# Kernel optimization log

Measured on AMD Instinct MI355X. Metric: run time of the kernel, lower is better.

The kernel has to match this reference:

```python
import jax, jax.numpy as jnp
import numpy as np

K = 16  # neighbors per point (no self-loop)


def _knn_idx(pos, k):
    # pos: (N, 3). Squared euclidean pairwise distances via the ||a-b||^2 expansion.
    n = pos.shape[0]
    sq = jnp.sum(pos * pos, axis=1)                      # (N,)
    d = sq[:, None] + sq[None, :] - 2.0 * (pos @ pos.T)  # (N, N)
    # exclude self (loop=False in torch_cluster.knn_graph)
    diag = jnp.arange(n)
    d = d.at[diag, diag].set(jnp.inf)
    _, idx = jax.lax.top_k(-d, k)                        # k smallest distances -> (N, k)
    return idx


def setup_inputs() -> dict:
    key = jax.random.key(0)
    ks = jax.random.split(key, 6)
    N, C, D = 16384, 64, 64
    x = jax.random.normal(ks[0], (N, C), dtype=jnp.float32)
    pos = jax.random.normal(ks[1], (N, 3), dtype=jnp.float32)
    W1 = jax.random.normal(ks[2], (2 * C, D), dtype=jnp.float32) * 0.08
    b1 = jax.random.normal(ks[3], (D,), dtype=jnp.float32) * 0.02
    W2 = jax.random.normal(ks[4], (D, D), dtype=jnp.float32) * 0.12
    b2 = jax.random.normal(ks[5], (D,), dtype=jnp.float32) * 0.02
    return {"x": x, "pos": pos, "W1": W1, "b1": b1, "W2": W2, "b2": b2}


def reference(x, pos, W1, b1, W2, b2):
    # EdgeConv: for each center i with k-NN neighbors j:
    #   e_ij = MLP([x_i, x_j - x_i]);  out_i = max_j e_ij
    idx = _knn_idx(pos, K)                               # (N, K) int32
    x_j = x[idx]                                         # (N, K, C) gather
    x_i = x[:, None, :]                                  # (N, 1, C)
    ef = jnp.concatenate(
        [jnp.broadcast_to(x_i, x_j.shape), x_j - x_i], axis=-1
    )                                                    # (N, K, 2C)
    h = jax.nn.relu(jnp.einsum("nkc,cd->nkd", ef, W1) + b1)
    h = jnp.einsum("nkd,de->nke", h, W2) + b2            # (N, K, D)
    # each node has exactly K incoming edges -> scatter_max == max over K axis
    return jnp.max(h, axis=1)                            # (N, D)
```

## Files before the change

kernel.cpp:

```cpp
#include <hip/hip_runtime.h>
#include <hip/hip_bf16.h>


#define NPTS 16384
#define CH 64

#define GLO  (-4.5f)
#define GH   0.28125f
#define INVH 3.5555555556f
#define GDIM 32
#define GCELLS (GDIM * GDIM * GDIM)

typedef __attribute__((ext_vector_type(8))) short short8;
typedef __attribute__((ext_vector_type(4))) float floatx4;

__device__ __forceinline__ unsigned short f2bf(float f) {
    unsigned u = __float_as_uint(f);
    u += 0x7FFFu + ((u >> 16) & 1u);
    return (unsigned short)(u >> 16);
}
__device__ __forceinline__ float bf2f(unsigned short u) {
    return __uint_as_float(((unsigned)u) << 16);
}
__device__ __forceinline__ unsigned wave_iscan(unsigned x) {
    x += (unsigned)__builtin_amdgcn_update_dpp(0, (int)x, 0x111, 0xF, 0xF, true);
    x += (unsigned)__builtin_amdgcn_update_dpp(0, (int)x, 0x112, 0xF, 0xF, true);
    x += (unsigned)__builtin_amdgcn_update_dpp(0, (int)x, 0x114, 0xF, 0xF, true);
    x += (unsigned)__builtin_amdgcn_update_dpp(0, (int)x, 0x118, 0xF, 0xF, true);
    x += (unsigned)__builtin_amdgcn_update_dpp(0, (int)x, 0x142, 0xA, 0xF, true);
    x += (unsigned)__builtin_amdgcn_update_dpp(0, (int)x, 0x143, 0xC, 0xF, true);
    return x;
}
__device__ __forceinline__ int cell_of(float x, float y, float z) {
    int cx = (int)floorf((x - GLO) * INVH);
    int cy = (int)floorf((y - GLO) * INVH);
    int cz = (int)floorf((z - GLO) * INVH);
    cx = min(max(cx, 0), GDIM - 1);
    cy = min(max(cy, 0), GDIM - 1);
    cz = min(max(cz, 0), GDIM - 1);
    return (cz * GDIM + cy) * GDIM + cx;
}

__global__ __launch_bounds__(256) void count_prep_kernel(const float* __restrict__ pos,
                                                         int* __restrict__ counts,
                                                         const float* __restrict__ x,
                                                         const float* __restrict__ W1,
                                                         const float* __restrict__ b1,
                                                         float* __restrict__ vout,
                                                         unsigned short* __restrict__ ubuf) {
    __shared__ unsigned short Wct[128 * 72];
    __shared__ unsigned short Abuf[64 * 72];
    __shared__ float Wraw[128 * 64];

    const int t = threadIdx.x;
    if (blockIdx.x < 64) {
        const int i = blockIdx.x * 256 + t;
        atomicAdd(&counts[cell_of(pos[i * 3], pos[i * 3 + 1], pos[i * 3 + 2])], 1);
        return;
    }
    const int bid  = blockIdx.x - 64;
    const int lane = t & 63;
    const int w    = t >> 6;

    {
        const float4* W1v = (const float4*)W1;
        float4* Wr4 = (float4*)Wraw;
#pragma unroll
        for (int i = 0; i < 8; ++i) Wr4[i * 256 + t] = W1v[i * 256 + t];
    }
    __syncthreads();
    {
        const int n = t & 127;
        const int ks = (t >> 7) * 32;
#pragma unroll
        for (int i = 0; i < 32; ++i) {
            const int k = ks + i;
            float val;
            if (n < 64) val = Wraw[k * 64 + n] - Wraw[(64 + k) * 64 + n];
            else        val = Wraw[(64 + k) * 64 + (n - 64)];
            Wct[n * 72 + k] = f2bf(val);
        }
    }
    {
        const int col = t & 63;
#pragma unroll
        for (int i = 0; i < 16; ++i) {
            const int r2 = (t >> 6) + 4 * i;
            const int gp = bid * 64 + r2;
            Abuf[r2 * 72 + col] = f2bf(x[(size_t)gp * CH + col]);
        }
    }
    __syncthreads();

    const int m16 = lane & 15;
    const int q   = lane >> 4;

    floatx4 acc[8];
#pragma unroll
    for (int nt = 0; nt < 8; ++nt) acc[nt] = (floatx4){0.f, 0.f, 0.f, 0.f};

#pragma unroll
    for (int kk = 0; kk < 64; kk += 32) {
        const short8 a = *(const short8*)(Abuf + (w * 16 + m16) * 72 + kk + q * 8);
#pragma unroll
        for (int nt = 0; nt < 8; ++nt) {
            const short8 b = *(const short8*)(Wct + (nt * 16 + m16) * 72 + kk + q * 8);
            acc[nt] = __builtin_amdgcn_mfma_f32_16x16x32_bf16(a, b, acc[nt], 0, 0, 0);
        }
    }

#pragma unroll
    for (int nt = 0; nt < 8; ++nt) {
        const int n = nt * 16 + m16;
#pragma unroll
        for (int r = 0; r < 4; ++r) {
            const int gp = bid * 64 + w * 16 + q * 4 + r;
            if (n < 64) vout[(size_t)gp * CH + n] = acc[nt][r] + b1[n];
            else        ubuf[(size_t)gp * CH + (n - 64)] = f2bf(acc[nt][r]);
        }
    }
}

__global__ __launch_bounds__(1024) void scan_kernel(const int* __restrict__ counts,
                                                    int* __restrict__ starts,
                                                    int* __restrict__ cursor) {
    __shared__ int lds[1024];
    const int t = threadIdx.x;
    int4 v[8];
    const int4* c4 = (const int4*)counts + t * 8;
#pragma unroll
    for (int i = 0; i < 8; ++i) v[i] = c4[i];
    int sum = 0;
#pragma unroll
    for (int i = 0; i < 8; ++i) sum += v[i].x + v[i].y + v[i].z + v[i].w;
    lds[t] = sum;
    __syncthreads();
    for (int off = 1; off < 1024; off <<= 1) {
        int x = 0;
        if (t >= off) x = lds[t - off];
        __syncthreads();
        lds[t] += x;
        __syncthreads();
    }
    int pre = (t == 0) ? 0 : lds[t - 1];
    int4* s4 = (int4*)starts + t * 8;
    int4* u4 = (int4*)cursor + t * 8;
#pragma unroll
    for (int i = 0; i < 8; ++i) {
        int4 o;
        o.x = pre; pre += v[i].x;
        o.y = pre; pre += v[i].y;
        o.z = pre; pre += v[i].z;
        o.w = pre; pre += v[i].w;
        s4[i] = o;
        u4[i] = o;
    }
    if (t == 1023) starts[GCELLS] = pre;
}

__global__ __launch_bounds__(256) void grid_scatter_kernel(const float* __restrict__ pos,
                                                           int* __restrict__ cursor,
                                                           float4* __restrict__ spos,
                                                           unsigned short* __restrict__ sidx) {
    const int i = blockIdx.x * 256 + threadIdx.x;
    const float a = pos[i * 3], b = pos[i * 3 + 1], c = pos[i * 3 + 2];
    const int dst = atomicAdd(&cursor[cell_of(a, b, c)], 1);
    spos[dst] = make_float4(a, b, c, a * a + b * b + c * c);
    sidx[dst] = (unsigned short)i;
}

#define SENT 0xFF800000FFFFFFFFULL
#define NB 4

__global__ __launch_bounds__(64) void knn_grid_kernel(const float4* __restrict__ spos,
                                                      const unsigned short* __restrict__ sidx,
                                                      const int* __restrict__ starts,
                                                      unsigned short* __restrict__ knn_out) {
    __shared__ int lds_ex[64];
    __shared__ int lds_st[64];
    __shared__ unsigned long long buf[64];
    const int lane = threadIdx.x;
    const int sq   = blockIdx.x;

    const float4 qv = spos[sq];
    const float qx = qv.x, qy = qv.y, qz = qv.z, sqi = qv.w;
    const int qrow = (int)sidx[sq];
    const int cix = min(max((int)floorf((qx - GLO) * INVH), 0), GDIM - 1);
    const int ciy = min(max((int)floorf((qy - GLO) * INVH), 0), GDIM - 1);
    const int ciz = min(max((int)floorf((qz - GLO) * INVH), 0), GDIM - 1);

    unsigned long long list = SENT;
    float tau = __uint_as_float(0x7F800000u);
    bool first = true;
    int nbuf = 0;

    auto do_flush = [&]() {
        unsigned long long ck = (lane < nbuf) ? buf[lane] : SENT;
#pragma unroll
        for (int k = 2; k <= 64; k <<= 1) {
#pragma unroll
            for (int jj = k >> 1; jj >= 1; jj >>= 1) {
                const unsigned long long o = __shfl_xor(ck, jj);
                const bool takeMin = (((lane & k) == 0) == ((lane & jj) == 0));
                const unsigned long long mn = (ck < o) ? ck : o;
                const unsigned long long mx = (ck < o) ? o : ck;
                ck = takeMin ? mn : mx;
            }
        }
        const unsigned long long cv = __shfl(ck, 31 - lane);
        unsigned long long m = SENT;
        if (lane < 16) m = list;
        else if (lane < 32) m = cv;
#pragma unroll
        for (int jj = 16; jj >= 1; jj >>= 1) {
            const unsigned long long o = __shfl_xor(m, jj);
            const unsigned long long mn = (m < o) ? m : o;
            const unsigned long long mx = (m < o) ? o : m;
            m = ((lane & jj) == 0) ? mn : mx;
        }
        list = m;
        const unsigned thi = (unsigned)__builtin_amdgcn_readlane(
            (int)(unsigned)(list >> 32), 15);
        const unsigned fb = (thi >= 0x80000000u) ? (thi & 0x7FFFFFFFu) : ~thi;
        tau = __uint_as_float(fb);
        nbuf = 0;
    };

    int pax = 1, pbx = 0, pay = 1, pby = 0, paz = 1, pbz = 0;

    for (int s = 1; s < GDIM + 1; ++s) {
        const int ax = max(cix - s, 0), bx = min(cix + s, GDIM - 1);
        const int ay = max(ciy - s, 0), by = min(ciy + s, GDIM - 1);
        const int az = max(ciz - s, 0), bz = min(ciz + s, GDIM - 1);
        const int dy = by - ay + 1, dz = bz - az + 1;
        const int npair = dy * dz;
        const float invdy = 1.0f / (float)dy;

        for (int pb = 0; pb < npair; pb += 64) {
            const int pair = pb + lane;
            int stA = 0, lenA = 0, stB = 0, lenB = 0;
            if (pair < npair) {
                const int czo = (int)(((float)pair + 0.5f) * invdy);
                const int cyo = pair - czo * dy;
                const int cy = ay + cyo, cz = az + czo;
                const int rowb = (cz * GDIM + cy) * GDIM;
                const bool inner = cy >= pay && cy <= pby && cz >= paz && cz <= pbz;
                const int bA = inner ? (pax - 1) : bx;
                if (bA >= ax) {
                    stA  = starts[rowb + ax];
                    lenA = starts[rowb + bA + 1] - stA;
                }
                if (inner) {
                    const int aB = pbx + 1;
                    if (bx >= aB) {
                        stB  = starts[rowb + aB];
                        lenB = starts[rowb + bx + 1] - stB;
                    }
                }
            }
#pragma unroll
            for (int setsel = 0; setsel < 2; ++setsel) {
                const int st  = setsel ? stB  : stA;
                const int len = setsel ? lenB : lenA;
                if (__ballot(len > 0) == 0ULL) continue;
                const unsigned pfx = wave_iscan((unsigned)len);
                const int T = __builtin_amdgcn_readlane((int)pfx, 63);
                lds_ex[lane] = (int)pfx - len;
                lds_st[lane] = st;

                for (int b0 = 0; b0 < T; b0 += 64 * NB) {
                    float4 pts[NB];
                    int    jor[NB];
                    bool   act[NB];
                    bool   live[NB];
#pragma unroll
                    for (int nb = 0; nb < NB; ++nb) {
                        const int bb = b0 + nb * 64;
                        live[nb] = bb < T;
                        act[nb] = false;
                        if (live[nb]) {
                            const int p = bb + lane;
                            int j = 0;
#pragma unroll
                            for (int stp = 32; stp >= 1; stp >>= 1) {
                                const int m = j + stp;
                                if (lds_ex[m] <= p) j = m;
                            }
                            int idx = lds_st[j] + (p - lds_ex[j]);
                            idx = min(idx, NPTS - 1);
                            act[nb] = p < T;
                            pts[nb] = spos[idx];
                            jor[nb] = (int)sidx[idx];
                        }
                    }
#pragma unroll
                    for (int nb = 0; nb < NB; ++nb) {
                        if (!live[nb]) continue;
                        const float dot = fmaf(qx, pts[nb].x,
                                               fmaf(qy, pts[nb].y, qz * pts[nb].z));
                        const float d = fmaf(-2.0f, dot, sqi + pts[nb].w);

                        if (first) {
                            first = false;
                            unsigned kd = __float_as_uint(d);
                            kd = ((int)kd < 0) ? ~kd : (kd | 0x80000000u);
                            unsigned long long key =
                                (((unsigned long long)kd) << 32) | (unsigned)jor[nb];
                            if (!(act[nb] && jor[nb] != qrow)) key = SENT;
#pragma unroll
                            for (int k = 2; k <= 64; k <<= 1) {
#pragma unroll
                                for (int jj = k >> 1; jj >= 1; jj >>= 1) {
                                    const unsigned long long o = __shfl_xor(key, jj);
                                    const bool takeMin =
                                        (((lane & k) == 0) == ((lane & jj) == 0));
                                    const unsigned long long mn = (key < o) ? key : o;
                                    const unsigned long long mx = (key < o) ? o : key;
                                    key = takeMin ? mn : mx;
                                }
                            }
                            list = key;
                            const unsigned thi = (unsigned)__builtin_amdgcn_readlane(
                                (int)(unsigned)(list >> 32), 15);
                            const unsigned fb =
                                (thi >= 0x80000000u) ? (thi & 0x7FFFFFFFu) : ~thi;
                            tau = __uint_as_float(fb);
                            continue;
                        }

                        const bool cand = act[nb] && (jor[nb] != qrow) && (d <= tau);
                        const unsigned long long mask = __ballot(cand);
                        if (mask) {
                            const int cnt = __popcll(mask);
                            if (nbuf + cnt > 64) do_flush();
                            if (cand) {
                                unsigned kd = __float_as_uint(d);
                                kd = ((int)kd < 0) ? ~kd : (kd | 0x80000000u);
                                const unsigned long long key =
                                    (((unsigned long long)kd) << 32) | (unsigned)jor[nb];
                                const int rank =
                                    __popcll(mask & ((1ULL << lane) - 1ULL));
                                buf[nbuf + rank] = key;
                            }
                            nbuf += cnt;
                        }
                    }
                }
            }
        }

        if (nbuf) do_flush();

        const float BIG = 1e30f;
        float dout = BIG;
        if (ax > 0)        dout = fminf(dout, qx - (GLO + ax * GH));
        if (bx < GDIM - 1) dout = fminf(dout, (GLO + (bx + 1) * GH) - qx);
        if (ay > 0)        dout = fminf(dout, qy - (GLO + ay * GH));
        if (by < GDIM - 1) dout = fminf(dout, (GLO + (by + 1) * GH) - qy);
        if (az > 0)        dout = fminf(dout, qz - (GLO + az * GH));
        if (bz < GDIM - 1) dout = fminf(dout, (GLO + (bz + 1) * GH) - qz);
        if (dout * dout > tau + 1e-4f) break;
        if (ax == 0 && bx == GDIM - 1 && ay == 0 && by == GDIM - 1 &&
            az == 0 && bz == GDIM - 1) break;
        pax = ax; pbx = bx; pay = ay; pby = by; paz = az; pbz = bz;
    }

    if (lane < 16)
        knn_out[qrow * 16 + lane] = (unsigned short)(list & 0xFFFFULL);
}

__global__ __launch_bounds__(256) void edge_kernel(const unsigned short* __restrict__ ubuf,
                                                   const float* __restrict__ W2,
                                                   const float* __restrict__ b2,
                                                   const unsigned short* __restrict__ knn,
                                                   float* __restrict__ out) {
    __shared__ unsigned short h[128 * 72];
    __shared__ unsigned short W2t[64 * 72];

    const int t    = threadIdx.x;
    const int lane = t & 63;
    const int w    = t >> 6;

    {
        const int n = t & 63;
        const int kb = (t >> 6) * 16;
#pragma unroll
        for (int i = 0; i < 16; ++i) {
            const int k = kb + i;
            W2t[n * 72 + k] = f2bf(W2[k * 64 + n]);
        }
    }
    {
        const int k = t >> 4;
        const int c = t & 15;
#pragma unroll
        for (int i = 0; i < 8; ++i) {
            const int gn = blockIdx.x * 8 + i;
            const int gj = (int)knn[gn * 16 + k];
            const float4  vv = ((const float4*)(out + (size_t)gn * CH))[c];
            const ushort4 uu = ((const ushort4*)(ubuf + (size_t)gj * CH))[c];
            ushort4 hv;
            hv.x = f2bf(fmaxf(vv.x + bf2f(uu.x), 0.f));
            hv.y = f2bf(fmaxf(vv.y + bf2f(uu.y), 0.f));
            hv.z = f2bf(fmaxf(vv.z + bf2f(uu.z), 0.f));
            hv.w = f2bf(fmaxf(vv.w + bf2f(uu.w), 0.f));
            const int r2 = i * 16 + k;
            *(ushort4*)(h + r2 * 72 + c * 4) = hv;
        }
    }
    __syncthreads();

    const int m16 = lane & 15;
    const int q   = lane >> 4;

    floatx4 acc[2][4];
#pragma unroll
    for (int i = 0; i < 2; ++i)
#pragma unroll
        for (int nt = 0; nt < 4; ++nt) acc[i][nt] = (floatx4){0.f, 0.f, 0.f, 0.f};

#pragma unroll
    for (int kk = 0; kk < 64; kk += 32) {
        const short8 a0 = *(const short8*)(h + ((w * 2 + 0) * 16 + m16) * 72 + kk + q * 8);
        const short8 a1 = *(const short8*)(h + ((w * 2 + 1) * 16 + m16) * 72 + kk + q * 8);
#pragma unroll
        for (int nt = 0; nt < 4; ++nt) {
            const short8 b = *(const short8*)(W2t + (nt * 16 + m16) * 72 + kk + q * 8);
            acc[0][nt] = __builtin_amdgcn_mfma_f32_16x16x32_bf16(a0, b, acc[0][nt], 0, 0, 0);
            acc[1][nt] = __builtin_amdgcn_mfma_f32_16x16x32_bf16(a1, b, acc[1][nt], 0, 0, 0);
        }
    }

#pragma unroll
    for (int i = 0; i < 2; ++i) {
        const int mt = w * 2 + i;
        const int gn = blockIdx.x * 8 + mt;
#pragma unroll
        for (int nt = 0; nt < 4; ++nt) {
            float m0 = fmaxf(fmaxf(acc[i][nt][0], acc[i][nt][1]),
                             fmaxf(acc[i][nt][2], acc[i][nt][3]));
            m0 = fmaxf(m0, __shfl_xor(m0, 16));
            m0 = fmaxf(m0, __shfl_xor(m0, 32));
            if (lane < 16)
                out[(size_t)gn * CH + nt * 16 + lane] = m0 + b2[nt * 16 + lane];
        }
    }
}

extern "C" void kernel_launch(void* const* d_in, const int* in_sizes, int n_in,
                              void* d_out, int out_size, void* d_ws, size_t ws_size,
                              hipStream_t stream) {
    const float* x   = (const float*)d_in[0];
    const float* pos = (const float*)d_in[1];
    const float* W1  = (const float*)d_in[2];
    const float* b1  = (const float*)d_in[3];
    const float* W2  = (const float*)d_in[4];
    const float* b2  = (const float*)d_in[5];
    float* out = (float*)d_out;

    char* ws = (char*)d_ws;
    unsigned short* knn  = (unsigned short*)ws;
    unsigned short* ubuf = (unsigned short*)(ws + 524288);
    int*    counts = (int*)(ws + 2621440);
    int*    starts = (int*)(ws + 2752512);
    int*    cursor = (int*)(ws + 2883600);
    float4* spos   = (float4*)(ws + 3014672);
    unsigned short* sidx = (unsigned short*)(ws + 3276816);

    hipMemsetAsync(counts, 0, GCELLS * sizeof(int), stream);
    count_prep_kernel<<<320, 256, 0, stream>>>(pos, counts, x, W1, b1, out, ubuf);
    scan_kernel<<<1, 1024, 0, stream>>>(counts, starts, cursor);
    grid_scatter_kernel<<<NPTS / 256, 256, 0, stream>>>(pos, cursor, spos, sidx);
    knn_grid_kernel<<<NPTS, 64, 0, stream>>>(spos, sidx, starts, knn);
    edge_kernel<<<NPTS / 8, 256, 0, stream>>>(ubuf, W2, b2, knn, out);
}
```

Measured before the change: 151.2 us.

## Fuse kNN with edge MLP, merge scan with scatter, precompute W2t

The edge MLP second layer and max-reduction now run inside the kNN kernel: each wave gathers its 16 neighbor features from the in-register candidate list and runs the MFMAs directly, so the knn index buffer round-trip and the separate edge kernel launch go away. The scan kernel switches from an LDS Hillis-Steele loop to a wave scan plus per-wave sums, and absorbs the grid scatter, which drops one launch. W2 transpose/bf16 conversion moves to an extra block of the prep kernel. The risks are a single-block scatter with only 1024 threads doing 16K atomics serially, and a two-wave kNN block layout that may change occupancy.

```diff
diff --git a/kernel.cpp b/kernel.cpp
--- a/kernel.cpp
+++ b/kernel.cpp
@@ -46,8 +46,10 @@
                                                          const float* __restrict__ x,
                                                          const float* __restrict__ W1,
                                                          const float* __restrict__ b1,
+                                                         const float* __restrict__ W2,
                                                          float* __restrict__ vout,
-                                                         unsigned short* __restrict__ ubuf) {
+                                                         unsigned short* __restrict__ ubuf,
+                                                         unsigned short* __restrict__ W2t) {
     __shared__ unsigned short Wct[128 * 72];
     __shared__ unsigned short Abuf[64 * 72];
     __shared__ float Wraw[128 * 64];
@@ -56,6 +58,13 @@
     if (blockIdx.x < 64) {
         const int i = blockIdx.x * 256 + t;
         atomicAdd(&counts[cell_of(pos[i * 3], pos[i * 3 + 1], pos[i * 3 + 2])], 1);
+        return;
+    }
+    if (blockIdx.x == 320) {
+        for (int i = t; i < 4096; i += 256) {
+            const int n = i >> 6, k = i & 63;
+            W2t[n * 64 + k] = f2bf(W2[k * 64 + n]);
+        }
         return;
     }
     const int bid  = blockIdx.x - 64;
@@ -121,11 +130,17 @@
     }
 }
 
-__global__ __launch_bounds__(1024) void scan_kernel(const int* __restrict__ counts,
-                                                    int* __restrict__ starts,
-                                                    int* __restrict__ cursor) {
-    __shared__ int lds[1024];
-    const int t = threadIdx.x;
+__global__ __launch_bounds__(1024) void scan_scatter_kernel(const float* __restrict__ pos,
+                                                            const int* __restrict__ counts,
+                                                            int* __restrict__ starts,
+                                                            int* __restrict__ cursor,
+                                                            float4* __restrict__ spos,
+                                                            unsigned short* __restrict__ sidx) {
+    __shared__ int wsum[16];
+    const int t    = threadIdx.x;
+    const int lane = t & 63;
+    const int wv   = t >> 6;
+
     int4 v[8];
     const int4* c4 = (const int4*)counts + t * 8;
 #pragma unroll
@@ -133,16 +148,14 @@
     int sum = 0;
 #pragma unroll
     for (int i = 0; i < 8; ++i) sum += v[i].x + v[i].y + v[i].z + v[i].w;
-    lds[t] = sum;
+
+    const unsigned incl = wave_iscan((unsigned)sum);
+    if (lane == 63) wsum[wv] = (int)incl;
     __syncthreads();
-    for (int off = 1; off < 1024; off <<= 1) {
-        int x = 0;
-        if (t >= off) x = lds[t - off];
-        __syncthreads();
-        lds[t] += x;
-        __syncthreads();
-    }
-    int pre = (t == 0) ? 0 : lds[t - 1];
+    int base = (int)incl - sum;
+    for (int k = 0; k < wv; ++k) base += wsum[k];
+
+    int pre = base;
     int4* s4 = (int4*)starts + t * 8;
     int4* u4 = (int4*)cursor + t * 8;
 #pragma unroll
@@ -156,31 +169,35 @@
         u4[i] = o;
     }
     if (t == 1023) starts[GCELLS] = pre;
-}
-
-__global__ __launch_bounds__(256) void grid_scatter_kernel(const float* __restrict__ pos,
-                                                           int* __restrict__ cursor,
-                                                           float4* __restrict__ spos,
-                                                           unsigned short* __restrict__ sidx) {
-    const int i = blockIdx.x * 256 + threadIdx.x;
-    const float a = pos[i * 3], b = pos[i * 3 + 1], c = pos[i * 3 + 2];
-    const int dst = atomicAdd(&cursor[cell_of(a, b, c)], 1);
-    spos[dst] = make_float4(a, b, c, a * a + b * b + c * c);
-    sidx[dst] = (unsigned short)i;
+    __syncthreads();
+
+    for (int i = t; i < NPTS; i += 1024) {
+        const float a = pos[i * 3], b = pos[i * 3 + 1], c = pos[i * 3 + 2];
+        const int dst = atomicAdd(&cursor[cell_of(a, b, c)], 1);
+        spos[dst] = make_float4(a, b, c, a * a + b * b + c * c);
+        sidx[dst] = (unsigned short)i;
+    }
 }
 
 #define SENT 0xFF800000FFFFFFFFULL
 #define NB 4
 
-__global__ __launch_bounds__(64) void knn_grid_kernel(const float4* __restrict__ spos,
-                                                      const unsigned short* __restrict__ sidx,
-                                                      const int* __restrict__ starts,
-                                                      unsigned short* __restrict__ knn_out) {
-    __shared__ int lds_ex[64];
-    __shared__ int lds_st[64];
-    __shared__ unsigned long long buf[64];
-    const int lane = threadIdx.x;
-    const int sq   = blockIdx.x;
+__global__ __launch_bounds__(128) void knn_edge_kernel(const float4* __restrict__ spos,
+                                                       const unsigned short* __restrict__ sidx,
+                                                       const int* __restrict__ starts,
+                                                       const unsigned short* __restrict__ ubuf,
+                                                       const unsigned short* __restrict__ W2t,
+                                                       const float* __restrict__ b2,
+                                                       float* __restrict__ out) {
+    __shared__ int lds_ex[128];
+    __shared__ int lds_st[128];
+    __shared__ unsigned long long bufs[128];
+    const int lane  = threadIdx.x & 63;
+    const int w     = threadIdx.x >> 6;
+    int* ex = lds_ex + w * 64;
+    int* st_ = lds_st + w * 64;
+    unsigned long long* buf = bufs + w * 64;
+    const int sq = blockIdx.x * 2 + w;
 
     const float4 qv = spos[sq];
     const float qx = qv.x, qy = qv.y, qz = qv.z, sqi = qv.w;
@@ -265,8 +282,8 @@
                 if (__ballot(len > 0) == 0ULL) continue;
                 const unsigned pfx = wave_iscan((unsigned)len);
                 const int T = __builtin_amdgcn_readlane((int)pfx, 63);
-                lds_ex[lane] = (int)pfx - len;
-                lds_st[lane] = st;
+                ex[lane] = (int)pfx - len;
+                st_[lane] = st;
 
                 for (int b0 = 0; b0 < T; b0 += 64 * NB) {
                     float4 pts[NB];
@@ -284,9 +301,9 @@
 #pragma unroll
                             for (int stp = 32; stp >= 1; stp >>= 1) {
                                 const int m = j + stp;
-                                if (lds_ex[m] <= p) j = m;
+                                if (ex[m] <= p) j = m;
                             }
-                            int idx = lds_st[j] + (p - lds_ex[j]);
+                            int idx = st_[j] + (p - ex[j]);
                             idx = min(idx, NPTS - 1);
                             act[nb] = p < T;
                             pts[nb] = spos[idx];
@@ -365,84 +382,53 @@
         pax = ax; pbx = bx; pay = ay; pby = by; paz = az; pbz = bz;
     }
 
-    if (lane < 16)
-        knn_out[qrow * 16 + lane] = (unsigned short)(list & 0xFFFFULL);
-}
-
-__global__ __launch_bounds__(256) void edge_kernel(const unsigned short* __restrict__ ubuf,
-                                                   const float* __restrict__ W2,
-                                                   const float* __restrict__ b2,
-                                                   const unsigned short* __restrict__ knn,
-                                                   float* __restrict__ out) {
-    __shared__ unsigned short h[128 * 72];
-    __shared__ unsigned short W2t[64 * 72];
-
-    const int t    = threadIdx.x;
-    const int lane = t & 63;
-    const int w    = t >> 6;
-
     {
-        const int n = t & 63;
-        const int kb = (t >> 6) * 16;
-#pragma unroll
-        for (int i = 0; i < 16; ++i) {
-            const int k = kb + i;
-            W2t[n * 72 + k] = f2bf(W2[k * 64 + n]);
-        }
-    }
-    {
-        const int k = t >> 4;
-        const int c = t & 15;
-#pragma unroll
-        for (int i = 0; i < 8; ++i) {
-            const int gn = blockIdx.x * 8 + i;
-            const int gj = (int)knn[gn * 16 + k];
-            const float4  vv = ((const float4*)(out + (size_t)gn * CH))[c];
-            const ushort4 uu = ((const ushort4*)(ubuf + (size_t)gj * CH))[c];
-            ushort4 hv;
-            hv.x = f2bf(fmaxf(vv.x + bf2f(uu.x), 0.f));
-            hv.y = f2bf(fmaxf(vv.y + bf2f(uu.y), 0.f));
-            hv.z = f2bf(fmaxf(vv.z + bf2f(uu.z), 0.f));
-            hv.w = f2bf(fmaxf(vv.w + bf2f(uu.w), 0.f));
-            const int r2 = i * 16 + k;
-            *(ushort4*)(h + r2 * 72 + c * 4) = hv;
-        }
-    }
-    __syncthreads();
-
-    const int m16 = lane & 15;
-    const int q   = lane >> 4;
-
-    floatx4 acc[2][4];
-#pragma unroll
-    for (int i = 0; i < 2; ++i)
-#pragma unroll
-        for (int nt = 0; nt < 4; ++nt) acc[i][nt] = (floatx4){0.f, 0.f, 0.f, 0.f};
-
-#pragma unroll
-    for (int kk = 0; kk < 64; kk += 32) {
-        const short8 a0 = *(const short8*)(h + ((w * 2 + 0) * 16 + m16) * 72 + kk + q * 8);
-        const short8 a1 = *(const short8*)(h + ((w * 2 + 1) * 16 + m16) * 72 + kk + q * 8);
+        const int m16 = lane & 15;
+        const int q   = lane >> 4;
+        const int j   = (int)(unsigned)(__shfl(list, m16) & 0xFFFFULL);
+
+        short8 hfrag[2];
+#pragma unroll
+        for (int kk2 = 0; kk2 < 2; ++kk2) {
+            const int kk = kk2 * 32;
+            const float*  vp = out  + (size_t)qrow * CH + kk + q * 8;
+            const ushort4 u0 = *(const ushort4*)(ubuf + (size_t)j * CH + kk + q * 8);
+            const ushort4 u1 = *(const ushort4*)(ubuf + (size_t)j * CH + kk + q * 8 + 4);
+            const float4 v0 = *(const float4*)(vp);
+            const float4 v1 = *(const float4*)(vp + 4);
+            short8 h;
+            h[0] = (short)f2bf(fmaxf(v0.x + bf2f(u0.x), 0.f));
+            h[1] = (short)f2bf(fmaxf(v0.y + bf2f(u0.y), 0.f));
+            h[2] = (short)f2bf(fmaxf(v0.z + bf2f(u0.z), 0.f));
+            h[3] = (short)f2bf(fmaxf(v0.w + bf2f(u0.w), 0.f));
+            h[4] = (short)f2bf(fmaxf(v1.x + bf2f(u1.x), 0.f));
+            h[5] = (short)f2bf(fmaxf(v1.y + bf2f(u1.y), 0.f));
+            h[6] = (short)f2bf(fmaxf(v1.z + bf2f(u1.z), 0.f));
+            h[7] = (short)f2bf(fmaxf(v1.w + bf2f(u1.w), 0.f));
+            hfrag[kk2] = h;
+        }
+
+        floatx4 acc[4];
+#pragma unroll
+        for (int nt = 0; nt < 4; ++nt) acc[nt] = (floatx4){0.f, 0.f, 0.f, 0.f};
+#pragma unroll
+        for (int kk2 = 0; kk2 < 2; ++kk2) {
+#pragma unroll
+            for (int nt = 0; nt < 4; ++nt) {
+                const short8 b =
+                    *(const short8*)(W2t + (nt * 16 + m16) * 64 + kk2 * 32 + q * 8);
+                acc[nt] = __builtin_amdgcn_mfma_f32_16x16x32_bf16(hfrag[kk2], b,
+                                                                  acc[nt], 0, 0, 0);
+            }
+        }
 #pragma unroll
         for (int nt = 0; nt < 4; ++nt) {
-            const short8 b = *(const short8*)(W2t + (nt * 16 + m16) * 72 + kk + q * 8);
-            acc[0][nt] = __builtin_amdgcn_mfma_f32_16x16x32_bf16(a0, b, acc[0][nt], 0, 0, 0);
-            acc[1][nt] = __builtin_amdgcn_mfma_f32_16x16x32_bf16(a1, b, acc[1][nt], 0, 0, 0);
-        }
-    }
-
-#pragma unroll
-    for (int i = 0; i < 2; ++i) {
-        const int mt = w * 2 + i;
-        const int gn = blockIdx.x * 8 + mt;
-#pragma unroll
-        for (int nt = 0; nt < 4; ++nt) {
-            float m0 = fmaxf(fmaxf(acc[i][nt][0], acc[i][nt][1]),
-                             fmaxf(acc[i][nt][2], acc[i][nt][3]));
+            float m0 = fmaxf(fmaxf(acc[nt][0], acc[nt][1]),
+                             fmaxf(acc[nt][2], acc[nt][3]));
             m0 = fmaxf(m0, __shfl_xor(m0, 16));
             m0 = fmaxf(m0, __shfl_xor(m0, 32));
             if (lane < 16)
-                out[(size_t)gn * CH + nt * 16 + lane] = m0 + b2[nt * 16 + lane];
+                out[(size_t)qrow * CH + nt * 16 + lane] = m0 + b2[nt * 16 + lane];
         }
     }
 }
@@ -459,18 +445,19 @@
     float* out = (float*)d_out;
 
     char* ws = (char*)d_ws;
-    unsigned short* knn  = (unsigned short*)ws;
     unsigned short* ubuf = (unsigned short*)(ws + 524288);
     int*    counts = (int*)(ws + 2621440);
     int*    starts = (int*)(ws + 2752512);
     int*    cursor = (int*)(ws + 2883600);
     float4* spos   = (float4*)(ws + 3014672);
     unsigned short* sidx = (unsigned short*)(ws + 3276816);
+    unsigned short* W2t  = (unsigned short*)(ws + 3309584);
 
     hipMemsetAsync(counts, 0, GCELLS * sizeof(int), stream);
-    count_prep_kernel<<<320, 256, 0, stream>>>(pos, counts, x, W1, b1, out, ubuf);
-    scan_kernel<<<1, 1024, 0, stream>>>(counts, starts, cursor);
-    grid_scatter_kernel<<<NPTS / 256, 256, 0, stream>>>(pos, cursor, spos, sidx);
-    knn_grid_kernel<<<NPTS, 64, 0, stream>>>(spos, sidx, starts, knn);
-    edge_kernel<<<NPTS / 8, 256, 0, stream>>>(ubuf, W2, b2, knn, out);
-}
+    count_prep_kernel<<<321, 256, 0, stream>>>(pos, counts, x, W1, b1, W2,
+                                               out, ubuf, W2t);
+    scan_scatter_kernel<<<1, 1024, 0, stream>>>(pos, counts, starts, cursor,
+                                                spos, sidx);
+    knn_edge_kernel<<<NPTS / 2, 128, 0, stream>>>(spos, sidx, starts, ubuf,
+                                                  W2t, b2, out);
+}
```

After: 211.9 us. 40.1% more time.

## Process four sorted queries per wave in grid kNN, sharing candidate loads

Applied to the files above, without the earlier changes.

Each kNN wavefront now handles four consecutive grid-sorted query points instead of one. It scans the union cell box around their cells and reuses every loaded candidate point across all four queries, each with its own top-16 list, threshold and buffer. The goal is to cut redundant global loads and cell-range setup per query, and to launch a quarter as many blocks. In exchange the shared search box is larger, the wave runs until all four queries finish, and the four-candidate batching and first-batch seeding of the threshold are removed. Register and LDS use also rise.

```diff
diff --git a/kernel.cpp b/kernel.cpp
--- a/kernel.cpp
+++ b/kernel.cpp
@@ -170,7 +170,7 @@
 }
 
 #define SENT 0xFF800000FFFFFFFFULL
-#define NB 4
+#define QPW 4
 
 __global__ __launch_bounds__(64) void knn_grid_kernel(const float4* __restrict__ spos,
                                                       const unsigned short* __restrict__ sidx,
@@ -178,24 +178,40 @@
                                                       unsigned short* __restrict__ knn_out) {
     __shared__ int lds_ex[64];
     __shared__ int lds_st[64];
-    __shared__ unsigned long long buf[64];
+    __shared__ unsigned long long bufs[QPW * 64];
     const int lane = threadIdx.x;
-    const int sq   = blockIdx.x;
-
-    const float4 qv = spos[sq];
-    const float qx = qv.x, qy = qv.y, qz = qv.z, sqi = qv.w;
-    const int qrow = (int)sidx[sq];
-    const int cix = min(max((int)floorf((qx - GLO) * INVH), 0), GDIM - 1);
-    const int ciy = min(max((int)floorf((qy - GLO) * INVH), 0), GDIM - 1);
-    const int ciz = min(max((int)floorf((qz - GLO) * INVH), 0), GDIM - 1);
-
-    unsigned long long list = SENT;
-    float tau = __uint_as_float(0x7F800000u);
-    bool first = true;
-    int nbuf = 0;
-
-    auto do_flush = [&]() {
-        unsigned long long ck = (lane < nbuf) ? buf[lane] : SENT;
+    const int sq0  = blockIdx.x * QPW;
+
+    float qx[QPW], qy[QPW], qz[QPW], sqi[QPW];
+    int qrow[QPW];
+    int cminx = GDIM, cmaxx = -1, cminy = GDIM, cmaxy = -1, cminz = GDIM, cmaxz = -1;
+#pragma unroll
+    for (int r = 0; r < QPW; ++r) {
+        const float4 qv = spos[sq0 + r];
+        qx[r] = qv.x; qy[r] = qv.y; qz[r] = qv.z; sqi[r] = qv.w;
+        qrow[r] = (int)sidx[sq0 + r];
+        const int cx = min(max((int)floorf((qv.x - GLO) * INVH), 0), GDIM - 1);
+        const int cy = min(max((int)floorf((qv.y - GLO) * INVH), 0), GDIM - 1);
+        const int cz = min(max((int)floorf((qv.z - GLO) * INVH), 0), GDIM - 1);
+        cminx = min(cminx, cx); cmaxx = max(cmaxx, cx);
+        cminy = min(cminy, cy); cmaxy = max(cmaxy, cy);
+        cminz = min(cminz, cz); cmaxz = max(cmaxz, cz);
+    }
+
+    unsigned long long list[QPW];
+    float tau[QPW];
+    int nbuf[QPW];
+    bool done[QPW];
+#pragma unroll
+    for (int r = 0; r < QPW; ++r) {
+        list[r] = SENT;
+        tau[r]  = __uint_as_float(0x7F800000u);
+        nbuf[r] = 0;
+        done[r] = false;
+    }
+
+    auto do_flush = [&](int r) {
+        unsigned long long ck = (lane < nbuf[r]) ? bufs[r * 64 + lane] : SENT;
 #pragma unroll
         for (int k = 2; k <= 64; k <<= 1) {
 #pragma unroll
@@ -209,7 +225,7 @@
         }
         const unsigned long long cv = __shfl(ck, 31 - lane);
         unsigned long long m = SENT;
-        if (lane < 16) m = list;
+        if (lane < 16) m = list[r];
         else if (lane < 32) m = cv;
 #pragma unroll
         for (int jj = 16; jj >= 1; jj >>= 1) {
@@ -218,20 +234,20 @@
             const unsigned long long mx = (m < o) ? o : m;
             m = ((lane & jj) == 0) ? mn : mx;
         }
-        list = m;
+        list[r] = m;
         const unsigned thi = (unsigned)__builtin_amdgcn_readlane(
-            (int)(unsigned)(list >> 32), 15);
+            (int)(unsigned)(list[r] >> 32), 15);
         const unsigned fb = (thi >= 0x80000000u) ? (thi & 0x7FFFFFFFu) : ~thi;
-        tau = __uint_as_float(fb);
-        nbuf = 0;
+        tau[r] = __uint_as_float(fb);
+        nbuf[r] = 0;
     };
 
     int pax = 1, pbx = 0, pay = 1, pby = 0, paz = 1, pbz = 0;
 
     for (int s = 1; s < GDIM + 1; ++s) {
-        const int ax = max(cix - s, 0), bx = min(cix + s, GDIM - 1);
-        const int ay = max(ciy - s, 0), by = min(ciy + s, GDIM - 1);
-        const int az = max(ciz - s, 0), bz = min(ciz + s, GDIM - 1);
+        const int ax = max(cminx - s, 0), bx = min(cmaxx + s, GDIM - 1);
+        const int ay = max(cminy - s, 0), by = min(cmaxy + s, GDIM - 1);
+        const int az = max(cminz - s, 0), bz = min(cmaxz + s, GDIM - 1);
         const int dy = by - ay + 1, dz = bz - az + 1;
         const int npair = dy * dz;
         const float invdy = 1.0f / (float)dy;
@@ -268,105 +284,77 @@
                 lds_ex[lane] = (int)pfx - len;
                 lds_st[lane] = st;
 
-                for (int b0 = 0; b0 < T; b0 += 64 * NB) {
-                    float4 pts[NB];
-                    int    jor[NB];
-                    bool   act[NB];
-                    bool   live[NB];
-#pragma unroll
-                    for (int nb = 0; nb < NB; ++nb) {
-                        const int bb = b0 + nb * 64;
-                        live[nb] = bb < T;
-                        act[nb] = false;
-                        if (live[nb]) {
-                            const int p = bb + lane;
-                            int j = 0;
-#pragma unroll
-                            for (int stp = 32; stp >= 1; stp >>= 1) {
-                                const int m = j + stp;
-                                if (lds_ex[m] <= p) j = m;
-                            }
-                            int idx = lds_st[j] + (p - lds_ex[j]);
-                            idx = min(idx, NPTS - 1);
-                            act[nb] = p < T;
-                            pts[nb] = spos[idx];
-                            jor[nb] = (int)sidx[idx];
-                        }
+                for (int b0 = 0; b0 < T; b0 += 64) {
+                    const int p = b0 + lane;
+                    int j = 0;
+#pragma unroll
+                    for (int stp = 32; stp >= 1; stp >>= 1) {
+                        const int m = j + stp;
+                        if (lds_ex[m] <= p) j = m;
                     }
-#pragma unroll
-                    for (int nb = 0; nb < NB; ++nb) {
-                        if (!live[nb]) continue;
-                        const float dot = fmaf(qx, pts[nb].x,
-                                               fmaf(qy, pts[nb].y, qz * pts[nb].z));
-                        const float d = fmaf(-2.0f, dot, sqi + pts[nb].w);
-
-                        if (first) {
-                            first = false;
-                            unsigned kd = __float_as_uint(d);
-                            kd = ((int)kd < 0) ? ~kd : (kd | 0x80000000u);
-                            unsigned long long key =
-                                (((unsigned long long)kd) << 32) | (unsigned)jor[nb];
-                            if (!(act[nb] && jor[nb] != qrow)) key = SENT;
-#pragma unroll
-                            for (int k = 2; k <= 64; k <<= 1) {
-#pragma unroll
-                                for (int jj = k >> 1; jj >= 1; jj >>= 1) {
-                                    const unsigned long long o = __shfl_xor(key, jj);
-                                    const bool takeMin =
-                                        (((lane & k) == 0) == ((lane & jj) == 0));
-                                    const unsigned long long mn = (key < o) ? key : o;
-                                    const unsigned long long mx = (key < o) ? o : key;
-                                    key = takeMin ? mn : mx;
-                                }
-                            }
-                            list = key;
-                            const unsigned thi = (unsigned)__builtin_amdgcn_readlane(
-                                (int)(unsigned)(list >> 32), 15);
-                            const unsigned fb =
-                                (thi >= 0x80000000u) ? (thi & 0x7FFFFFFFu) : ~thi;
-                            tau = __uint_as_float(fb);
-                            continue;
-                        }
-
-                        const bool cand = act[nb] && (jor[nb] != qrow) && (d <= tau);
+                    int idx = lds_st[j] + (p - lds_ex[j]);
+                    idx = min(idx, NPTS - 1);
+                    const bool active = p < T;
+                    const float4 pt = spos[idx];
+                    const int jorig = (int)sidx[idx];
+
+#pragma unroll
+                    for (int r = 0; r < QPW; ++r) {
+                        if (done[r]) continue;
+                        const float dot = fmaf(qx[r], pt.x,
+                                               fmaf(qy[r], pt.y, qz[r] * pt.z));
+                        const float d = fmaf(-2.0f, dot, sqi[r] + pt.w);
+                        const bool cand = active && (jorig != qrow[r]) &&
+                                          (d <= tau[r]);
                         const unsigned long long mask = __ballot(cand);
                         if (mask) {
                             const int cnt = __popcll(mask);
-                            if (nbuf + cnt > 64) do_flush();
+                            if (nbuf[r] + cnt > 64) do_flush(r);
                             if (cand) {
                                 unsigned kd = __float_as_uint(d);
                                 kd = ((int)kd < 0) ? ~kd : (kd | 0x80000000u);
                                 const unsigned long long key =
-                                    (((unsigned long long)kd) << 32) | (unsigned)jor[nb];
+                                    (((unsigned long long)kd) << 32) |
+                                    (unsigned)jorig;
                                 const int rank =
                                     __popcll(mask & ((1ULL << lane) - 1ULL));
-                                buf[nbuf + rank] = key;
+                                bufs[r * 64 + nbuf[r] + rank] = key;
                             }
-                            nbuf += cnt;
+                            nbuf[r] += cnt;
                         }
                     }
                 }
             }
         }
 
-        if (nbuf) do_flush();
-
-        const float BIG = 1e30f;
-        float dout = BIG;
-        if (ax > 0)        dout = fminf(dout, qx - (GLO + ax * GH));
-        if (bx < GDIM - 1) dout = fminf(dout, (GLO + (bx + 1) * GH) - qx);
-        if (ay > 0)        dout = fminf(dout, qy - (GLO + ay * GH));
-        if (by < GDIM - 1) dout = fminf(dout, (GLO + (by + 1) * GH) - qy);
-        if (az > 0)        dout = fminf(dout, qz - (GLO + az * GH));
-        if (bz < GDIM - 1) dout = fminf(dout, (GLO + (bz + 1) * GH) - qz);
-        if (dout * dout > tau + 1e-4f) break;
-        if (ax == 0 && bx == GDIM - 1 && ay == 0 && by == GDIM - 1 &&
-            az == 0 && bz == GDIM - 1) break;
+        bool alldone = true;
+        const bool fullcube = (ax == 0 && bx == GDIM - 1 && ay == 0 &&
+                               by == GDIM - 1 && az == 0 && bz == GDIM - 1);
+#pragma unroll
+        for (int r = 0; r < QPW; ++r) {
+            if (!done[r]) {
+                if (nbuf[r]) do_flush(r);
+                const float BIG = 1e30f;
+                float dout = BIG;
+                if (ax > 0)        dout = fminf(dout, qx[r] - (GLO + ax * GH));
+                if (bx < GDIM - 1) dout = fminf(dout, (GLO + (bx + 1) * GH) - qx[r]);
+                if (ay > 0)        dout = fminf(dout, qy[r] - (GLO + ay * GH));
+                if (by < GDIM - 1) dout = fminf(dout, (GLO + (by + 1) * GH) - qy[r]);
+                if (az > 0)        dout = fminf(dout, qz[r] - (GLO + az * GH));
+                if (bz < GDIM - 1) dout = fminf(dout, (GLO + (bz + 1) * GH) - qz[r]);
+                if (dout * dout > tau[r] + 1e-4f || fullcube) done[r] = true;
+                else alldone = false;
+            }
+        }
+        if (alldone) break;
         pax = ax; pbx = bx; pay = ay; pby = by; paz = az; pbz = bz;
     }
 
-    if (lane < 16)
-        knn_out[qrow * 16 + lane] = (unsigned short)(list & 0xFFFFULL);
+#pragma unroll
+    for (int r = 0; r < QPW; ++r)
+        if (lane < 16)
+            knn_out[qrow[r] * 16 + lane] =
+                (unsigned short)(list[r] & 0xFFFFULL);
 }
 
 __global__ __launch_bounds__(256) void edge_kernel(const unsigned short* __restrict__ ubuf,
@@ -471,6 +459,6 @@
     count_prep_kernel<<<320, 256, 0, stream>>>(pos, counts, x, W1, b1, out, ubuf);
     scan_kernel<<<1, 1024, 0, stream>>>(counts, starts, cursor);
     grid_scatter_kernel<<<NPTS / 256, 256, 0, stream>>>(pos, cursor, spos, sidx);
-    knn_grid_kernel<<<NPTS, 64, 0, stream>>>(spos, sidx, starts, knn);
+    knn_grid_kernel<<<NPTS / QPW, 64, 0, stream>>>(spos, sidx, starts, knn);
     edge_kernel<<<NPTS / 8, 256, 0, stream>>>(ubuf, W2, b2, knn, out);
 }
```

After: 300.5 us. +98.7%, slower.
